# Performance work log

Measured on AMD Instinct MI355X. Metric: run time of the kernel, lower is better.

The kernel has to match this reference:

```python
import jax, jax.numpy as jnp
import numpy as np

NH = 16      # neighborhood size
MD = 128     # model_dim
FF = 512     # ff_dim
HEADS = 4
DH = MD // HEADS
LN100 = float(np.log(100.0))

def leaky(x):
    return jnp.where(x >= 0, x, 0.2 * x)

def layer_norm(x, g, b, eps=1e-5):
    m = jnp.mean(x, axis=-1, keepdims=True)
    v = jnp.var(x, axis=-1, keepdims=True)
    return (x - m) * jax.lax.rsqrt(v + eps) * g + b

def setup_inputs() -> dict:
    key = jax.random.key(0)
    ks = jax.random.split(key, 16)
    b, t = 4, 4096
    def lin(k, i, o):
        return (jax.random.normal(k, (i, o), jnp.float32) / np.sqrt(i)).astype(jnp.float32)
    return {
        "x": jax.random.normal(ks[0], (b, t, MD), jnp.float32),
        "coords": jax.random.uniform(ks[1], (b, t, 2), jnp.float32),
        "w_v": lin(ks[2], MD, MD),
        "w_q": lin(ks[3], MD, MD),
        "w_k": lin(ks[4], MD, MD),
        "pe_w1": lin(ks[5], 2, MD), "pe_b1": jnp.zeros((MD,), jnp.float32),
        "pe_w2": lin(ks[6], MD, MD), "pe_b2": jnp.zeros((MD,), jnp.float32),
        "logit_scale": jnp.full((HEADS, 1, 1), float(np.log(10.0)), jnp.float32),
        "w_o": lin(ks[7], MD, MD), "b_o": jnp.zeros((MD,), jnp.float32),
        "mlp_nh_w1": lin(ks[8], MD, FF), "mlp_nh_b1": jnp.zeros((FF,), jnp.float32),
        "mlp_nh_w2": lin(ks[9], FF, 1), "mlp_nh_b2": jnp.zeros((1,), jnp.float32),
        "mlp_u_w1": lin(ks[10], MD * NH, MD * NH), "mlp_u_b1": jnp.zeros((MD * NH,), jnp.float32),
        "mlp_u_w2": lin(ks[11], MD * NH, MD * NH), "mlp_u_b2": jnp.zeros((MD * NH,), jnp.float32),
        "ln1_g": jnp.ones((MD,), jnp.float32), "ln1_b": jnp.zeros((MD,), jnp.float32),
        "ln2_g": jnp.ones((MD,), jnp.float32), "ln2_b": jnp.zeros((MD,), jnp.float32),
        "ln3_g": jnp.ones((MD * NH,), jnp.float32), "ln3_b": jnp.zeros((MD * NH,), jnp.float32),
    }

def reference(x, coords, w_v, w_q, w_k, pe_w1, pe_b1, pe_w2, pe_b2,
              logit_scale, w_o, b_o, mlp_nh_w1, mlp_nh_b1, mlp_nh_w2, mlp_nh_b2,
              mlp_u_w1, mlp_u_b1, mlp_u_w2, mlp_u_b2,
              ln1_g, ln1_b, ln2_g, ln2_b, ln3_g, ln3_b):
    b, t, e = x.shape
    # --- nn_layer: nh nearest neighbors by Euclidean distance (cart=True) ---
    d2 = jnp.sum((coords[:, :, None, :] - coords[:, None, :, :]) ** 2, axis=-1)  # [b,t,t]
    _, idx = jax.lax.top_k(-d2, NH)                                              # [b,t,NH]
    xg = jax.vmap(lambda xb, ib: xb[ib])(x, idx)                                 # [b,t,NH,e]
    cg = jax.vmap(lambda cb, ib: cb[ib])(coords, idx)                            # [b,t,NH,2]
    cs = cg - coords[:, :, None, :]                                              # relative Cartesian coords
    # --- value projection on raw gathered features ---
    v = xg.reshape(b * t, NH, e) @ w_v                                           # [bt,NH,MD]
    # --- relative positional encoding (MLP on cs) ---
    pe = leaky(cs @ pe_w1 + pe_b1) @ pe_w2 + pe_b2                               # [b,t,NH,MD]
    h = layer_norm(xg + pe, ln1_g, ln1_b).reshape(b * t, NH, MD)
    q = h @ w_q
    k = h @ w_k
    # --- logit-scaled (cosine) multi-head attention over the neighborhood ---
    B = b * t
    qh = q.reshape(B, NH, HEADS, DH).transpose(0, 2, 1, 3)                       # [bt,H,NH,dh]
    kh = k.reshape(B, NH, HEADS, DH).transpose(0, 2, 1, 3)
    vh = v.reshape(B, NH, HEADS, DH).transpose(0, 2, 1, 3)
    qn = qh / jnp.clip(jnp.linalg.norm(qh, axis=-1, keepdims=True), 1e-6)
    kn = kh / jnp.clip(jnp.linalg.norm(kh, axis=-1, keepdims=True), 1e-6)
    scale = jnp.exp(jnp.minimum(logit_scale, LN100))                             # [H,1,1]
    logits = jnp.einsum('bhnd,bhmd->bhnm', qn, kn) * scale
    attn = jax.nn.softmax(logits, axis=-1)
    att_out = jnp.einsum('bhnm,bhmd->bhnd', attn, vh)
    att_out = att_out.transpose(0, 2, 1, 3).reshape(B, NH, MD) @ w_o + b_o
    # --- residual + norm + per-neighbor MLP (md -> ff -> 1, broadcast add) ---
    h = layer_norm(h + att_out, ln2_g, ln2_b)
    m = leaky(leaky(h @ mlp_nh_w1 + mlp_nh_b1) @ mlp_nh_w2 + mlp_nh_b2)          # [bt,NH,1]
    h = h + m
    # --- unfold neighborhood and mix ---
    h = h.reshape(b, t, NH * MD)
    h = layer_norm(h, ln3_g, ln3_b)
    h = leaky(leaky(h @ mlp_u_w1 + mlp_u_b1) @ mlp_u_w2 + mlp_u_b2)
    return h
```

## Files before the change

### kernel.cpp

```cpp
#include <hip/hip_runtime.h>
#include <hip/hip_bf16.h>
#include <stdint.h>

#define TLEN   4096
#define BATCH  4
#define BT     (BATCH*TLEN)
#define MDNH   2048
#define LN100F 4.605170185988092f

typedef __attribute__((ext_vector_type(8))) short bf16x8;
typedef __attribute__((ext_vector_type(4))) float f32x4;
typedef unsigned int u32;

__device__ __forceinline__ float leakyf(float v){ return v >= 0.f ? v : 0.2f*v; }
__device__ __forceinline__ short f2bf(float v){ __hip_bfloat16 h = __float2bfloat16(v); return *reinterpret_cast<short*>(&h); }
__device__ __forceinline__ float bf2f(short s){
  union { u32 u; float f; } cv; cv.u = ((u32)(unsigned short)s) << 16; return cv.f;
}
__device__ __forceinline__ int sw128(int row, int col){ return row*128 + (col ^ ((row&7)<<3)); }
__device__ __forceinline__ float redcol(float v){
  v += __shfl_xor(v,1); v += __shfl_xor(v,2); v += __shfl_xor(v,4); v += __shfl_xor(v,8);
  return v;
}

__global__ __launch_bounds__(256) void knn_kernel(const float* __restrict__ coords,
                                                  int* __restrict__ idx_out,
                                                  float* __restrict__ cs_out) {
  __shared__ float sc[TLEN*2];
  int blk = blockIdx.x;
  int bb  = blk >> 10;
  int q0  = (blk & 1023) << 2;
  const float4* cb4 = (const float4*)(coords + (size_t)bb*TLEN*2);
  for (int i = threadIdx.x; i < TLEN*2/4; i += 256) ((float4*)sc)[i] = cb4[i];
  __syncthreads();

  int wid  = threadIdx.x >> 6;
  int lane = threadIdx.x & 63;
  int q    = q0 + wid;
  float qx = sc[q*2], qy = sc[q*2+1];

  unsigned long long top[16];
#pragma unroll
  for (int j = 0; j < 16; ++j) top[j] = ~0ull;

  for (int c = lane; c < TLEN; c += 64) {
    float dx = __fsub_rn(sc[c*2],   qx);
    float dy = __fsub_rn(sc[c*2+1], qy);
    float d2 = __fadd_rn(__fmul_rn(dx,dx), __fmul_rn(dy,dy));
    unsigned long long key = ((unsigned long long)__float_as_uint(d2) << 32) | (unsigned)c;
    if (key < top[15]) {
#pragma unroll
      for (int j = 15; j >= 1; --j)
        top[j] = (key < top[j-1]) ? top[j-1] : ((key < top[j]) ? key : top[j]);
      top[0] = (key < top[0]) ? key : top[0];
    }
  }

  unsigned long long myres = 0;
  for (int k = 0; k < 16; ++k) {
    unsigned long long m = top[0];
#pragma unroll
    for (int s = 1; s < 64; s <<= 1) {
      unsigned long long o = __shfl_xor(m, s);
      m = (o < m) ? o : m;
    }
    if (lane == k) myres = m;
    if (top[0] == m) {
#pragma unroll
      for (int j = 0; j < 15; ++j) top[j] = top[j+1];
      top[15] = ~0ull;
    }
  }
  if (lane < 16) {
    int ci = (int)(unsigned)(myres & 0xffffffffull);
    size_t o = ((size_t)(bb*TLEN + q))*16 + lane;
    idx_out[o] = ci;
    cs_out[o*2+0] = __fsub_rn(sc[ci*2],   qx);
    cs_out[o*2+1] = __fsub_rn(sc[ci*2+1], qy);
  }
}

__global__ __launch_bounds__(256) void transpose_to_bf16(const float* __restrict__ in,
                                                         short* __restrict__ out,
                                                         int R, int C) {
  __shared__ float tile[32][33];
  int c0 = blockIdx.x*32, r0 = blockIdx.y*32;
  int tx = threadIdx.x & 31, ty = threadIdx.x >> 5;
  for (int i = ty; i < 32; i += 8) tile[i][tx] = in[(size_t)(r0+i)*C + c0+tx];
  __syncthreads();
  for (int i = ty; i < 32; i += 8) out[(size_t)(c0+i)*R + r0+tx] = f2bf(tile[tx][i]);
}

__device__ __forceinline__ void gemm128(const short* Asrc, short* sW,
                                        const short* __restrict__ Wt,
                                        f32x4 acc[8], int w, int lane, int tid) {
#pragma unroll
  for (int ph = 0; ph < 2; ++ph) {
    __syncthreads();
#pragma unroll
    for (int q = 0; q < 2; ++q) {
      int c = tid + 512*q;
      int row = c >> 3, slot = c & 7;
      uint4 wv = *(const uint4*)(Wt + (size_t)row*128 + ph*64 + slot*8);
      *(uint4*)&sW[row*64 + ((slot*8) ^ ((row&7)<<3))] = wv;
    }
    __syncthreads();
#pragma unroll
    for (int ks = 0; ks < 2; ++ks) {
      bf16x8 af = *(const bf16x8*)&Asrc[sw128(16*w + (lane&15),
                                              ph*64 + ks*32 + (lane>>4)*8)];
#pragma unroll
      for (int nf = 0; nf < 8; ++nf) {
        int wr = nf*16 + (lane&15);
        bf16x8 bv = *(const bf16x8*)&sW[wr*64 + ((ks*32 + (lane>>4)*8) ^ ((wr&7)<<3))];
        acc[nf] = __builtin_amdgcn_mfma_f32_16x16x32_bf16(af, bv, acc[nf], 0, 0, 0);
      }
    }
  }
}

__device__ __forceinline__ void frag_store(short* buf, const f32x4* acc, int w, int lane) {
  int rb = 16*w + (lane>>4)*4;
  int cc = lane & 15;
#pragma unroll
  for (int nf = 0; nf < 8; ++nf)
#pragma unroll
    for (int i = 0; i < 4; ++i)
      buf[sw128(rb+i, nf*16+cc)] = f2bf(acc[nf][i]);
}

__global__ __launch_bounds__(512) void token_mfma(
    const float* __restrict__ x, const int* __restrict__ idx, const float* __restrict__ cs,
    const short* __restrict__ wvt, const short* __restrict__ wqt, const short* __restrict__ wkt,
    const short* __restrict__ wot, const short* __restrict__ pew2t, const short* __restrict__ nhw1t,
    const float* __restrict__ pe_w1, const float* __restrict__ pe_b1, const float* __restrict__ pe_b2,
    const float* __restrict__ lscale, const float* __restrict__ b_o,
    const float* __restrict__ nh_b1, const float* __restrict__ nh_w2, const float* __restrict__ nh_b2,
    const float* __restrict__ ln1_g, const float* __restrict__ ln1_b,
    const float* __restrict__ ln2_g, const float* __restrict__ ln2_b,
    const float* __restrict__ ln3_g, const float* __restrict__ ln3_b,
    short* __restrict__ Hn) {
  __shared__ short sA[128*128];
  __shared__ short sB[128*128];
  __shared__ short sH[128*128];
  __shared__ short sV[128*128];
  __shared__ short sW[128*64];

  const int tid  = threadIdx.x;
  const int w    = tid >> 6;
  const int lane = tid & 63;
  const int cc   = lane & 15;
  const int kg   = lane >> 4;
  const int r0   = 16*w + kg*4;
  const int token = blockIdx.x*8 + w;
  const int batch = token >> 12;

  int myidx = 0; float mcsx = 0.f, mcsy = 0.f;
  if (lane < 16) {
    size_t o = (size_t)token*16 + lane;
    myidx = idx[o];
    mcsx  = cs[o*2];
    mcsy  = cs[o*2+1];
  }

#pragma unroll
  for (int p = 0; p < 4; ++p) {
    int c   = lane + 64*p;
    int rl  = c >> 4;
    int seg = c & 15;
    int xr  = __shfl(myidx, rl);
    const float* gp = x + ((size_t)batch*TLEN + xr)*128 + seg*8;
    float4 a = *(const float4*)gp;
    float4 b = *(const float4*)(gp+4);
    union { short h[8]; uint4 u; } pk;
    pk.h[0]=f2bf(a.x); pk.h[1]=f2bf(a.y); pk.h[2]=f2bf(a.z); pk.h[3]=f2bf(a.w);
    pk.h[4]=f2bf(b.x); pk.h[5]=f2bf(b.y); pk.h[6]=f2bf(b.z); pk.h[7]=f2bf(b.w);
    *(uint4*)&sA[sw128(16*w+rl, seg*8)] = pk.u;

    float cx = __shfl(mcsx, rl), cy = __shfl(mcsy, rl);
    int col0 = seg*8;
    float pw0[8], pw1[8], pb1[8];
    *(float4*)&pw0[0] = *(const float4*)(pe_w1 + col0);
    *(float4*)&pw0[4] = *(const float4*)(pe_w1 + col0 + 4);
    *(float4*)&pw1[0] = *(const float4*)(pe_w1 + 128 + col0);
    *(float4*)&pw1[4] = *(const float4*)(pe_w1 + 128 + col0 + 4);
    *(float4*)&pb1[0] = *(const float4*)(pe_b1 + col0);
    *(float4*)&pb1[4] = *(const float4*)(pe_b1 + col0 + 4);
    union { short h[8]; uint4 u; } pk2;
#pragma unroll
    for (int j = 0; j < 8; ++j) pk2.h[j] = f2bf(leakyf(cx*pw0[j] + cy*pw1[j] + pb1[j]));
    *(uint4*)&sB[sw128(16*w+rl, seg*8)] = pk2.u;
  }

  f32x4 acc[8];
  f32x4 h1v[8];

#pragma unroll
  for (int nf = 0; nf < 8; ++nf) { float b = pe_b2[nf*16+cc]; acc[nf] = (f32x4){b,b,b,b}; }
  gemm128(sB, sW, pew2t, acc, w, lane, tid);
  {
#pragma unroll
    for (int nf = 0; nf < 8; ++nf)
#pragma unroll
      for (int i = 0; i < 4; ++i)
        acc[nf][i] += bf2f(sA[sw128(r0+i, nf*16+cc)]);
    float sum[4] = {0,0,0,0}, ssq[4] = {0,0,0,0};
#pragma unroll
    for (int nf = 0; nf < 8; ++nf)
#pragma unroll
      for (int i = 0; i < 4; ++i) { float v = acc[nf][i]; sum[i] += v; ssq[i] += v*v; }
    float rstd[4], mean[4];
#pragma unroll
    for (int i = 0; i < 4; ++i) {
      float s = redcol(sum[i]), q2 = redcol(ssq[i]);
      mean[i] = s*(1.f/128.f);
      rstd[i] = rsqrtf(q2*(1.f/128.f) - mean[i]*mean[i] + 1e-5f);
    }
#pragma unroll
    for (int nf = 0; nf < 8; ++nf) {
      float g = ln1_g[nf*16+cc], b = ln1_b[nf*16+cc];
#pragma unroll
      for (int i = 0; i < 4; ++i) h1v[nf][i] = (acc[nf][i]-mean[i])*rstd[i]*g + b;
    }
  }
  frag_store(sH, h1v, w, lane);

#pragma unroll
  for (int nf = 0; nf < 8; ++nf) acc[nf] = (f32x4){0,0,0,0};
  gemm128(sA, sW, wvt, acc, w, lane, tid);
  frag_store(sV, acc, w, lane);

#pragma unroll
  for (int nf = 0; nf < 8; ++nf) acc[nf] = (f32x4){0,0,0,0};
  gemm128(sH, sW, wqt, acc, w, lane, tid);
#pragma unroll
  for (int h = 0; h < 4; ++h)
#pragma unroll
    for (int i = 0; i < 4; ++i) {
      float ss = acc[2*h][i]*acc[2*h][i] + acc[2*h+1][i]*acc[2*h+1][i];
      ss = redcol(ss);
      float inv = 1.f / fmaxf(sqrtf(ss), 1e-6f);
      acc[2*h][i] *= inv; acc[2*h+1][i] *= inv;
    }
  frag_store(sA, acc, w, lane);

#pragma unroll
  for (int nf = 0; nf < 8; ++nf) acc[nf] = (f32x4){0,0,0,0};
  gemm128(sH, sW, wkt, acc, w, lane, tid);
#pragma unroll
  for (int h = 0; h < 4; ++h)
#pragma unroll
    for (int i = 0; i < 4; ++i) {
      float ss = acc[2*h][i]*acc[2*h][i] + acc[2*h+1][i]*acc[2*h+1][i];
      ss = redcol(ss);
      float inv = 1.f / fmaxf(sqrtf(ss), 1e-6f);
      acc[2*h][i] *= inv; acc[2*h+1][i] *= inv;
    }
  frag_store(sB, acc, w, lane);

  {
    float* sPf = (float*)sB;
    float scl[4];
#pragma unroll
    for (int h = 0; h < 4; ++h) scl[h] = expf(fminf(lscale[h], LN100F));

    float lgt[4][4];
#pragma unroll
    for (int h = 0; h < 4; ++h) {
      bf16x8 qv[4];
#pragma unroll
      for (int s = 0; s < 4; ++s)
        qv[s] = *(const bf16x8*)&sA[sw128(16*w + cc, h*32 + s*8)];
#pragma unroll
      for (int kk = 0; kk < 4; ++kk) {
        int k = kg*4 + kk;
        float d = 0.f;
#pragma unroll
        for (int s = 0; s < 4; ++s) {
          bf16x8 kv = *(const bf16x8*)&sB[sw128(16*w + k, h*32 + s*8)];
#pragma unroll
          for (int j = 0; j < 8; ++j) d += bf2f(qv[s][j]) * bf2f(kv[j]);
        }
        lgt[h][kk] = d * scl[h];
      }
    }
#pragma unroll
    for (int h = 0; h < 4; ++h) {
      float m = fmaxf(fmaxf(lgt[h][0],lgt[h][1]), fmaxf(lgt[h][2],lgt[h][3]));
      m = fmaxf(m, __shfl_xor(m,16)); m = fmaxf(m, __shfl_xor(m,32));
      float e[4], s_ = 0.f;
#pragma unroll
      for (int kk = 0; kk < 4; ++kk) { e[kk] = expf(lgt[h][kk]-m); s_ += e[kk]; }
      s_ += __shfl_xor(s_,16); s_ += __shfl_xor(s_,32);
      float inv = 1.f/s_;
#pragma unroll
      for (int kk = 0; kk < 4; ++kk)
        sPf[(16*w + cc)*64 + h*16 + kg*4 + kk] = e[kk]*inv;
    }
    f32x4 av[8];
#pragma unroll
    for (int nf = 0; nf < 8; ++nf) av[nf] = (f32x4){0,0,0,0};
    for (int k = 0; k < 16; ++k) {
      float pv4[4][4];
#pragma unroll
      for (int i = 0; i < 4; ++i)
#pragma unroll
        for (int h = 0; h < 4; ++h)
          pv4[h][i] = sPf[(16*w + kg*4 + i)*64 + h*16 + k];
#pragma unroll
      for (int nf = 0; nf < 8; ++nf) {
        float vv = bf2f(sV[sw128(16*w + k, nf*16 + cc)]);
        int h = nf >> 1;
#pragma unroll
        for (int i = 0; i < 4; ++i) av[nf][i] += pv4[h][i] * vv;
      }
    }
    frag_store(sA, av, w, lane);
  }

#pragma unroll
  for (int nf = 0; nf < 8; ++nf) { float b = b_o[nf*16+cc]; acc[nf] = (f32x4){b,b,b,b}; }
  gemm128(sA, sW, wot, acc, w, lane, tid);
  {
#pragma unroll
    for (int nf = 0; nf < 8; ++nf)
#pragma unroll
      for (int i = 0; i < 4; ++i) acc[nf][i] += h1v[nf][i];
    float sum[4] = {0,0,0,0}, ssq[4] = {0,0,0,0};
#pragma unroll
    for (int nf = 0; nf < 8; ++nf)
#pragma unroll
      for (int i = 0; i < 4; ++i) { float v = acc[nf][i]; sum[i] += v; ssq[i] += v*v; }
    float rstd[4], mean[4];
#pragma unroll
    for (int i = 0; i < 4; ++i) {
      float s = redcol(sum[i]), q2 = redcol(ssq[i]);
      mean[i] = s*(1.f/128.f);
      rstd[i] = rsqrtf(q2*(1.f/128.f) - mean[i]*mean[i] + 1e-5f);
    }
#pragma unroll
    for (int nf = 0; nf < 8; ++nf) {
      float g = ln2_g[nf*16+cc], b = ln2_b[nf*16+cc];
#pragma unroll
      for (int i = 0; i < 4; ++i) h1v[nf][i] = (acc[nf][i]-mean[i])*rstd[i]*g + b;
    }
  }
  frag_store(sA, h1v, w, lane);

  float pm[4] = {0,0,0,0};
#pragma unroll
  for (int chn = 0; chn < 4; ++chn) {
#pragma unroll
    for (int nf = 0; nf < 8; ++nf) { float b = nh_b1[chn*128 + nf*16+cc]; acc[nf] = (f32x4){b,b,b,b}; }
    gemm128(sA, sW, nhw1t + (size_t)chn*128*128, acc, w, lane, tid);
#pragma unroll
    for (int nf = 0; nf < 8; ++nf) {
      float w2v = nh_w2[chn*128 + nf*16 + cc];
#pragma unroll
      for (int i = 0; i < 4; ++i) pm[i] += leakyf(acc[nf][i]) * w2v;
    }
  }
  {
    float b2 = nh_b2[0];
    float mval[4];
#pragma unroll
    for (int i = 0; i < 4; ++i) mval[i] = leakyf(redcol(pm[i]) + b2);
    float tsum = 0.f, tssq = 0.f;
#pragma unroll
    for (int nf = 0; nf < 8; ++nf)
#pragma unroll
      for (int i = 0; i < 4; ++i) {
        float h3 = h1v[nf][i] + mval[i];
        acc[nf][i] = h3;
        tsum += h3; tssq += h3*h3;
      }
#pragma unroll
    for (int s = 1; s < 64; s <<= 1) { tsum += __shfl_xor(tsum,s); tssq += __shfl_xor(tssq,s); }
    float mean = tsum*(1.f/2048.f);
    float rstd = rsqrtf(tssq*(1.f/2048.f) - mean*mean + 1e-5f);
#pragma unroll
    for (int nf = 0; nf < 8; ++nf)
#pragma unroll
      for (int i = 0; i < 4; ++i) acc[nf][i] = (acc[nf][i]-mean)*rstd;
  }
  frag_store(sB, acc, w, lane);

#pragma unroll
  for (int p = 0; p < 4; ++p) {
    int c   = lane + 64*p;
    int rl  = c >> 4;
    int seg = c & 15;
    bf16x8 hv = *(const bf16x8*)&sB[sw128(16*w+rl, seg*8)];
    float gv[8], bv[8];
    *(float4*)&gv[0] = *(const float4*)(ln3_g + rl*128 + seg*8);
    *(float4*)&gv[4] = *(const float4*)(ln3_g + rl*128 + seg*8 + 4);
    *(float4*)&bv[0] = *(const float4*)(ln3_b + rl*128 + seg*8);
    *(float4*)&bv[4] = *(const float4*)(ln3_b + rl*128 + seg*8 + 4);
    union { short h[8]; uint4 u; } pk;
#pragma unroll
    for (int j = 0; j < 8; ++j) pk.h[j] = f2bf(bf2f(hv[j])*gv[j] + bv[j]);
    *(uint4*)(Hn + (size_t)token*MDNH + rl*128 + seg*8) = pk.u;
  }
}

template<int OUT_BF16>
__global__ __launch_bounds__(256) void gemm_bias_leaky(
    const short* __restrict__ A, const short* __restrict__ Bt,
    const float* __restrict__ bias, void* __restrict__ Cout,
    int M, int N, int K) {
  __shared__ short sA[128*32];
  __shared__ short sB[128*32];
  int mt = M >> 7;
  int bm = blockIdx.x % mt, bn = blockIdx.x / mt;
  int brow = bm << 7, bcol = bn << 7;
  int tid  = threadIdx.x;
  int wid  = tid >> 6, lane = tid & 63;
  int wr = wid >> 1, wc = wid & 1;

  f32x4 acc[4][4];
#pragma unroll
  for (int m = 0; m < 4; ++m)
#pragma unroll
    for (int n = 0; n < 4; ++n) { acc[m][n][0]=0.f; acc[m][n][1]=0.f; acc[m][n][2]=0.f; acc[m][n][3]=0.f; }

  const short* Ab = A  + (size_t)brow*K;
  const short* Bb = Bt + (size_t)bcol*K;
  int ca = wid*128 + lane;
  int rA0 = ca >> 2,  sA0 = ca & 3;
  int rA1 = (ca+64) >> 2, sA1 = (ca+64) & 3;

  for (int k0 = 0; k0 < K; k0 += 32) {
    uint4 a0 = *(const uint4*)(Ab + (size_t)rA0*K + k0 + sA0*8);
    uint4 a1 = *(const uint4*)(Ab + (size_t)rA1*K + k0 + sA1*8);
    uint4 b0 = *(const uint4*)(Bb + (size_t)rA0*K + k0 + sA0*8);
    uint4 b1 = *(const uint4*)(Bb + (size_t)rA1*K + k0 + sA1*8);
    __syncthreads();
    *(uint4*)&sA[(size_t)ca*8]      = a0;
    *(uint4*)&sA[(size_t)(ca+64)*8] = a1;
    *(uint4*)&sB[(size_t)ca*8]      = b0;
    *(uint4*)&sB[(size_t)(ca+64)*8] = b1;
    __syncthreads();
    bf16x8 af[4], bfr[4];
#pragma unroll
    for (int m = 0; m < 4; ++m) af[m]  = *(bf16x8*)&sA[(wr*64 + m*16 + (lane&15))*32 + (lane>>4)*8];
#pragma unroll
    for (int n = 0; n < 4; ++n) bfr[n] = *(bf16x8*)&sB[(wc*64 + n*16 + (lane&15))*32 + (lane>>4)*8];
#pragma unroll
    for (int m = 0; m < 4; ++m)
#pragma unroll
      for (int n = 0; n < 4; ++n)
        acc[m][n] = __builtin_amdgcn_mfma_f32_16x16x32_bf16(af[m], bfr[n], acc[m][n], 0, 0, 0);
  }

  int lr = (lane >> 4) * 4, lc = lane & 15;
#pragma unroll
  for (int n = 0; n < 4; ++n) {
    int col = bcol + wc*64 + n*16 + lc;
    float bv = bias[col];
#pragma unroll
    for (int m = 0; m < 4; ++m) {
      int row0 = brow + wr*64 + m*16 + lr;
#pragma unroll
      for (int i = 0; i < 4; ++i) {
        float v = leakyf(acc[m][n][i] + bv);
        if (OUT_BF16) ((short*)Cout)[(size_t)(row0+i)*N + col] = f2bf(v);
        else          ((float*)Cout)[(size_t)(row0+i)*N + col] = v;
      }
    }
  }
}

extern "C" void kernel_launch(void* const* d_in, const int* in_sizes, int n_in,
                              void* d_out, int out_size, void* d_ws, size_t ws_size,
                              hipStream_t stream) {
  const float* x      = (const float*)d_in[0];
  const float* coords = (const float*)d_in[1];
  const float* w_v    = (const float*)d_in[2];
  const float* w_q    = (const float*)d_in[3];
  const float* w_k    = (const float*)d_in[4];
  const float* pe_w1  = (const float*)d_in[5];
  const float* pe_b1  = (const float*)d_in[6];
  const float* pe_w2  = (const float*)d_in[7];
  const float* pe_b2  = (const float*)d_in[8];
  const float* lscale = (const float*)d_in[9];
  const float* w_o    = (const float*)d_in[10];
  const float* b_o    = (const float*)d_in[11];
  const float* nh_w1  = (const float*)d_in[12];
  const float* nh_b1  = (const float*)d_in[13];
  const float* nh_w2  = (const float*)d_in[14];
  const float* nh_b2  = (const float*)d_in[15];
  const float* u_w1   = (const float*)d_in[16];
  const float* u_b1   = (const float*)d_in[17];
  const float* u_w2   = (const float*)d_in[18];
  const float* u_b2   = (const float*)d_in[19];
  const float* ln1_g  = (const float*)d_in[20];
  const float* ln1_b  = (const float*)d_in[21];
  const float* ln2_g  = (const float*)d_in[22];
  const float* ln2_b  = (const float*)d_in[23];
  const float* ln3_g  = (const float*)d_in[24];
  const float* ln3_b  = (const float*)d_in[25];

  char* ws = (char*)d_ws;
  int*   idxb = (int*)ws;
  float* csb  = (float*)(ws + (1ull<<20));
  short* wvt  = (short*)(ws + (3ull<<20));
  short* wqt  = (short*)(ws + (3ull<<20) + 32*1024);
  short* wkt  = (short*)(ws + (3ull<<20) + 64*1024);
  short* wot  = (short*)(ws + (3ull<<20) + 96*1024);
  short* pew2t= (short*)(ws + (3ull<<20) + 128*1024);
  short* nhw1t= (short*)(ws + (3ull<<20) + 160*1024);
  short* uw1t = (short*)(ws + (4ull<<20));
  short* uw2t = (short*)(ws + (12ull<<20));
  short* G1   = (short*)(ws + (20ull<<20));
  short* Hn   = (short*)d_out;

  dim3 t128(4,4), tnh(16,4), t2k(64,64);
  transpose_to_bf16<<<t128, 256, 0, stream>>>(w_v,   wvt,   128, 128);
  transpose_to_bf16<<<t128, 256, 0, stream>>>(w_q,   wqt,   128, 128);
  transpose_to_bf16<<<t128, 256, 0, stream>>>(w_k,   wkt,   128, 128);
  transpose_to_bf16<<<t128, 256, 0, stream>>>(w_o,   wot,   128, 128);
  transpose_to_bf16<<<t128, 256, 0, stream>>>(pe_w2, pew2t, 128, 128);
  transpose_to_bf16<<<tnh,  256, 0, stream>>>(nh_w1, nhw1t, 128, 512);
  transpose_to_bf16<<<t2k,  256, 0, stream>>>(u_w1,  uw1t,  MDNH, MDNH);
  transpose_to_bf16<<<t2k,  256, 0, stream>>>(u_w2,  uw2t,  MDNH, MDNH);

  knn_kernel<<<BT/4, 256, 0, stream>>>(coords, idxb, csb);

  token_mfma<<<BT/8, 512, 0, stream>>>(x, idxb, csb,
      wvt, wqt, wkt, wot, pew2t, nhw1t,
      pe_w1, pe_b1, pe_b2, lscale, b_o,
      nh_b1, nh_w2, nh_b2,
      ln1_g, ln1_b, ln2_g, ln2_b, ln3_g, ln3_b, Hn);

  int mt = BT/128, nt = MDNH/128;
  gemm_bias_leaky<1><<<mt*nt, 256, 0, stream>>>(Hn, uw1t, u_b1, G1, BT, MDNH, MDNH);
  gemm_bias_leaky<0><<<mt*nt, 256, 0, stream>>>(G1, uw2t, u_b2, (float*)d_out, BT, MDNH, MDNH);
}
```

Baseline: 1.215 ms.

## Load GEMM tiles directly into LDS and remap workgroups across XCDs

The two large 2048x2048 GEMMs now use global_load_lds to move A and B tiles straight from global memory into shared memory, bypassing registers. Workgroup IDs are also remapped so that consecutive tiles are spread across the 8 XCDs, improving L2 locality. The direct-to-LDS path drops the register staging and the VGPR stores, but the loop still has no double buffering. The new LDS layout must match the fragment read indexing, and the remap assumes the grid size is divisible by 8.

```diff
diff --git a/kernel.cpp b/kernel.cpp
--- a/kernel.cpp
+++ b/kernel.cpp
@@ -11,6 +11,8 @@
 typedef __attribute__((ext_vector_type(8))) short bf16x8;
 typedef __attribute__((ext_vector_type(4))) float f32x4;
 typedef unsigned int u32;
+#define AS1 __attribute__((address_space(1)))
+#define AS3 __attribute__((address_space(3)))
 
 __device__ __forceinline__ float leakyf(float v){ return v >= 0.f ? v : 0.2f*v; }
 __device__ __forceinline__ short f2bf(float v){ __hip_bfloat16 h = __float2bfloat16(v); return *reinterpret_cast<short*>(&h); }
@@ -404,14 +406,18 @@
 }
 
 template<int OUT_BF16>
-__global__ __launch_bounds__(256) void gemm_bias_leaky(
+__global__ __launch_bounds__(256) void gemm_m97(
     const short* __restrict__ A, const short* __restrict__ Bt,
     const float* __restrict__ bias, void* __restrict__ Cout,
     int M, int N, int K) {
   __shared__ short sA[128*32];
   __shared__ short sB[128*32];
   int mt = M >> 7;
-  int bm = blockIdx.x % mt, bn = blockIdx.x / mt;
+  int nwg = gridDim.x;
+  int q8 = nwg >> 3;
+  int wg = blockIdx.x;
+  int wgid = (wg & 7)*q8 + (wg >> 3);
+  int bm = wgid % mt, bn = wgid / mt;
   int brow = bm << 7, bcol = bn << 7;
   int tid  = threadIdx.x;
   int wid  = tid >> 6, lane = tid & 63;
@@ -421,24 +427,24 @@
 #pragma unroll
   for (int m = 0; m < 4; ++m)
 #pragma unroll
-    for (int n = 0; n < 4; ++n) { acc[m][n][0]=0.f; acc[m][n][1]=0.f; acc[m][n][2]=0.f; acc[m][n][3]=0.f; }
+    for (int n = 0; n < 4; ++n) acc[m][n] = (f32x4){0,0,0,0};
 
   const short* Ab = A  + (size_t)brow*K;
   const short* Bb = Bt + (size_t)bcol*K;
-  int ca = wid*128 + lane;
-  int rA0 = ca >> 2,  sA0 = ca & 3;
-  int rA1 = (ca+64) >> 2, sA1 = (ca+64) & 3;
+  int rowc0 = (wid*2)*16   + (lane>>2);
+  int rowc1 = (wid*2+1)*16 + (lane>>2);
+  int seg   = lane & 3;
 
   for (int k0 = 0; k0 < K; k0 += 32) {
-    uint4 a0 = *(const uint4*)(Ab + (size_t)rA0*K + k0 + sA0*8);
-    uint4 a1 = *(const uint4*)(Ab + (size_t)rA1*K + k0 + sA1*8);
-    uint4 b0 = *(const uint4*)(Bb + (size_t)rA0*K + k0 + sA0*8);
-    uint4 b1 = *(const uint4*)(Bb + (size_t)rA1*K + k0 + sA1*8);
     __syncthreads();
-    *(uint4*)&sA[(size_t)ca*8]      = a0;
-    *(uint4*)&sA[(size_t)(ca+64)*8] = a1;
-    *(uint4*)&sB[(size_t)ca*8]      = b0;
-    *(uint4*)&sB[(size_t)(ca+64)*8] = b1;
+    __builtin_amdgcn_global_load_lds((const AS1 u32*)(Ab + (size_t)rowc0*K + k0 + seg*8),
+                                     (AS3 u32*)(sA + wid*1024),       16, 0, 0);
+    __builtin_amdgcn_global_load_lds((const AS1 u32*)(Ab + (size_t)rowc1*K + k0 + seg*8),
+                                     (AS3 u32*)(sA + wid*1024 + 512), 16, 0, 0);
+    __builtin_amdgcn_global_load_lds((const AS1 u32*)(Bb + (size_t)rowc0*K + k0 + seg*8),
+                                     (AS3 u32*)(sB + wid*1024),       16, 0, 0);
+    __builtin_amdgcn_global_load_lds((const AS1 u32*)(Bb + (size_t)rowc1*K + k0 + seg*8),
+                                     (AS3 u32*)(sB + wid*1024 + 512), 16, 0, 0);
     __syncthreads();
     bf16x8 af[4], bfr[4];
 #pragma unroll
@@ -533,6 +539,6 @@
       ln1_g, ln1_b, ln2_g, ln2_b, ln3_g, ln3_b, Hn);
 
   int mt = BT/128, nt = MDNH/128;
-  gemm_bias_leaky<1><<<mt*nt, 256, 0, stream>>>(Hn, uw1t, u_b1, G1, BT, MDNH, MDNH);
-  gemm_bias_leaky<0><<<mt*nt, 256, 0, stream>>>(G1, uw2t, u_b2, (float*)d_out, BT, MDNH, MDNH);
-}
+  gemm_m97<1><<<mt*nt, 256, 0, stream>>>(Hn, uw1t, u_b1, G1, BT, MDNH, MDNH);
+  gemm_m97<0><<<mt*nt, 256, 0, stream>>>(G1, uw2t, u_b2, (float*)d_out, BT, MDNH, MDNH);
+}
```

New measurement: 1.246 ms. +2.5%, slower.
